# Kernel tuning notes

Measured on AMD Instinct MI355X. Metric: run time of the kernel, lower is better.

## Reference

```python
import jax, jax.numpy as jnp
import numpy as np

LS = (0, 1, 2, 3)                 # spherical-harmonic degrees of edge_attrs
DIMS = [2 * l + 1 for l in LS]    # [1,3,5,7], total 16
OFFS = np.cumsum([0] + DIMS)      # slice offsets into the SH axis
C = 128                           # node feature channels (128x0e)
C_DOWN = 64                       # node_feats_down_irreps = 64x0e
N_BESSEL = 8                      # edge_feats_irreps = 8x0e
AVG_NUM_NEIGHBORS = 10.0


def setup_inputs() -> dict:
    key = jax.random.key(0)
    ks = jax.random.split(key, 14)
    N, E = 10000, 100000
    node_attrs = jax.random.normal(ks[0], (N, 10), jnp.float32)
    node_feats = jax.random.normal(ks[1], (N, C), jnp.float32)
    edge_attrs = jax.random.normal(ks[2], (E, sum(DIMS)), jnp.float32)
    edge_feats = jax.random.normal(ks[3], (E, N_BESSEL), jnp.float32)
    edge_index = jax.random.randint(ks[4], (2, E), 0, N, dtype=jnp.int32)
    inv_c = 1.0 / np.sqrt(C)
    W_up = jax.random.normal(ks[5], (C, C), jnp.float32) * inv_c
    W_down = jax.random.normal(ks[6], (C, C_DOWN), jnp.float32) * inv_c
    W_skip = jax.random.normal(ks[7], (C, C), jnp.float32) * inv_c
    # FullyConnectedNet dims: [8 + 2*64] + 3*[256] + [weight_numel = 4*C]
    dims = [N_BESSEL + 2 * C_DOWN, 256, 256, 256, len(LS) * C]
    W_fc0 = jax.random.normal(ks[8], (dims[0], dims[1]), jnp.float32)
    W_fc1 = jax.random.normal(ks[9], (dims[1], dims[2]), jnp.float32)
    W_fc2 = jax.random.normal(ks[10], (dims[2], dims[3]), jnp.float32)
    W_fc3 = jax.random.normal(ks[11], (dims[3], dims[4]), jnp.float32)
    # final Linear(irreps_mid -> target): independent channel mixing per l
    W_out = jax.random.normal(ks[12], (len(LS), C, C), jnp.float32) * inv_c
    return dict(node_attrs=node_attrs, node_feats=node_feats, edge_attrs=edge_attrs,
                edge_feats=edge_feats, edge_index=edge_index,
                W_up=W_up, W_down=W_down, W_skip=W_skip,
                W_fc0=W_fc0, W_fc1=W_fc1, W_fc2=W_fc2, W_fc3=W_fc3, W_out=W_out)


def reference(node_attrs, node_feats, edge_attrs, edge_feats, edge_index,
              W_up, W_down, W_skip, W_fc0, W_fc1, W_fc2, W_fc3, W_out):
    sender = edge_index[0]
    receiver = edge_index[1]
    N = node_feats.shape[0]

    # skip connection (e3nn Linear on 0e channels)
    sc = node_feats @ W_skip                                   # [N, C]
    x_up = node_feats @ W_up                                   # [N, C]
    x_down = node_feats @ W_down                               # [N, 64]

    # radial weight network on augmented edge features
    aug = jnp.concatenate([edge_feats, x_down[sender], x_down[receiver]], axis=-1)  # [E, 136]
    h = aug
    for W in (W_fc0, W_fc1, W_fc2):
        h = jax.nn.silu(h @ (W / jnp.sqrt(jnp.asarray(W.shape[0], h.dtype))))
    tp_w = h @ (W_fc3 / jnp.sqrt(jnp.asarray(W_fc3.shape[0], h.dtype)))  # [E, 4*C]
    tp_w = tp_w.reshape(-1, len(LS), C)                        # [E, 4, C]

    # per-edge 'uvu' tensor product: 128x0e (gathered sender) x SH(lmax=3)
    xs = x_up[sender]                                          # [E, C]
    parts = []
    for i, l in enumerate(LS):
        Y = edge_attrs[:, OFFS[i]:OFFS[i + 1]]                 # [E, 2l+1]
        cg = 1.0 / np.sqrt(2 * l + 1)                          # w3j(0,l,l)
        part = (tp_w[:, i, :] * xs)[:, :, None] * (Y * cg)[:, None, :]  # [E, C, 2l+1]
        parts.append(part.reshape(part.shape[0], C * (2 * l + 1)))
    mji = jnp.concatenate(parts, axis=-1)                      # [E, C*16]

    # scatter-sum to receivers
    message = jax.ops.segment_sum(mji, receiver, num_segments=N)  # [N, C*16]

    # per-l channel-mixing linear, then / avg_num_neighbors, then reshape_irreps
    outs = []
    off = 0
    for i, l in enumerate(LS):
        d = 2 * l + 1
        blk = message[:, off:off + C * d].reshape(N, C, d)
        outs.append(jnp.einsum('ncd,ck->nkd', blk, W_out[i]))
        off += C * d
    out = jnp.concatenate(outs, axis=-1) / AVG_NUM_NEIGHBORS   # [N, C, 16]
    return out, sc
```

## Files before the change

kernel.cpp:

```cpp
#include <hip/hip_runtime.h>
#include <math.h>

using bf16x8 = __attribute__((ext_vector_type(8))) short;
using f32x4  = __attribute__((ext_vector_type(4))) float;

__device__ __forceinline__ float silu_f(float x) {
    float e = __expf(-x);
    float d = 1.f + e;
    return x * __builtin_amdgcn_rcpf(d);
}

__device__ __forceinline__ unsigned short f2bf(float x) {
    union { float f; unsigned u; } v; v.f = x;
    unsigned u = v.u;
    return (unsigned short)((u + 0x7FFFu + ((u >> 16) & 1u)) >> 16);
}
__device__ __forceinline__ unsigned f2bf2(float lo, float hi) {
    return (unsigned)f2bf(lo) | ((unsigned)f2bf(hi) << 16);
}
__device__ __forceinline__ float bf2f(unsigned short h) {
    union { unsigned u; float f; } v; v.u = ((unsigned)h) << 16;
    return v.f;
}

__global__ __launch_bounds__(256) void k_node_gemm(
    const float* __restrict__ A,
    const float* __restrict__ Wskip, const float* __restrict__ Wup, const float* __restrict__ Wdown,
    float* __restrict__ sc, float* __restrict__ xup, float* __restrict__ xdown, int N)
{
    __shared__ float As[64][129];
    const int t = threadIdx.x;
    const int n0 = blockIdx.x * 64;
    for (int i = t; i < 64 * 32; i += 256) {
        int r = i >> 5, c4 = i & 31;
        int n = n0 + r;
        float4 v = make_float4(0.f, 0.f, 0.f, 0.f);
        if (n < N) v = ((const float4*)(A + (size_t)n * 128))[c4];
        As[r][c4 * 4 + 0] = v.x; As[r][c4 * 4 + 1] = v.y;
        As[r][c4 * 4 + 2] = v.z; As[r][c4 * 4 + 3] = v.w;
    }
    __syncthreads();
    const int tc = t & 15, tr = t >> 4;
    const int col0 = blockIdx.y * 64 + tc * 4;
    const float* W; float* dst; int ldw, wc, ldd;
    if (col0 < 128)      { W = Wskip; ldw = 128; wc = col0;       dst = sc;    ldd = 128; }
    else if (col0 < 256) { W = Wup;   ldw = 128; wc = col0 - 128; dst = xup;   ldd = 128; }
    else                 { W = Wdown; ldw = 64;  wc = col0 - 256; dst = xdown; ldd = 64;  }
    float acc[4][4] = {};
    for (int k = 0; k < 128; k++) {
        float4 wv = *(const float4*)(W + (size_t)k * ldw + wc);
        float wvv[4] = {wv.x, wv.y, wv.z, wv.w};
        float av[4];
        #pragma unroll
        for (int ii = 0; ii < 4; ii++) av[ii] = As[tr * 4 + ii][k];
        #pragma unroll
        for (int ii = 0; ii < 4; ii++)
            #pragma unroll
            for (int jj = 0; jj < 4; jj++)
                acc[ii][jj] = fmaf(av[ii], wvv[jj], acc[ii][jj]);
    }
    #pragma unroll
    for (int ii = 0; ii < 4; ii++) {
        int n = n0 + tr * 4 + ii;
        if (n < N)
            *(float4*)(dst + (size_t)n * ldd + wc) =
                make_float4(acc[ii][0], acc[ii][1], acc[ii][2], acc[ii][3]);
    }
}

__global__ __launch_bounds__(256) void k_prep_w(
    const float* __restrict__ W, unsigned short* __restrict__ Wt,
    int Kin, int Kpad, int Nout, float scale)
{
    int i = blockIdx.x * 256 + threadIdx.x;
    if (i >= Nout * Kpad) return;
    int n = i / Kpad, k = i - n * Kpad;
    float v = (k < Kin) ? W[(size_t)k * Nout + n] * scale : 0.f;
    Wt[i] = f2bf(v);
}

#define MEB 128

__global__ __launch_bounds__(512, 2) void k_mlp_mfma(
    const float* __restrict__ ef, const int* __restrict__ eidx,
    const float* __restrict__ xdown,
    const unsigned short* __restrict__ Wt0, const unsigned short* __restrict__ Wt1,
    const unsigned short* __restrict__ Wt2, const unsigned short* __restrict__ Wt3,
    unsigned short* __restrict__ tp_w, int E, int eLo, int eHi)
{
    __shared__ unsigned short bufA[MEB][264];
    __shared__ unsigned short bufB[MEB][264];
    __shared__ int sE[MEB], rE[MEB];
    const int t = threadIdx.x;
    const int w = t >> 6, lane = t & 63;
    const int rA = lane & 15;
    const int kb = (lane >> 4) * 8;
    const int r0 = (lane >> 4) * 4;
    const int e0 = eLo + blockIdx.x * MEB;

    bf16x8 bw[16];
    f32x4 acc[8][2];

#define LOADW(WT, KPADW, NKS)                                                     \
    _Pragma("unroll")                                                             \
    for (int ks = 0; ks < NKS; ks++)                                              \
        _Pragma("unroll")                                                         \
        for (int nt = 0; nt < 2; nt++)                                            \
            bw[ks * 2 + nt] = *(const bf16x8*)&(WT)[(size_t)(w * 32 + nt * 16 + rA) * (KPADW) + ks * 32 + kb];

#define LMFMA(IN, NKS)                                                            \
    _Pragma("unroll")                                                             \
    for (int mt = 0; mt < 8; mt++)                                                \
        _Pragma("unroll")                                                         \
        for (int nt = 0; nt < 2; nt++)                                            \
            acc[mt][nt] = (f32x4){0.f, 0.f, 0.f, 0.f};                            \
    _Pragma("unroll")                                                             \
    for (int ks = 0; ks < NKS; ks++) {                                            \
        const int kk = ks * 32 + kb;                                              \
        bf16x8 afr[8];                                                            \
        _Pragma("unroll")                                                         \
        for (int mt = 0; mt < 8; mt++)                                            \
            afr[mt] = *(const bf16x8*)&IN[mt * 16 + rA][kk];                      \
        _Pragma("unroll")                                                         \
        for (int mt = 0; mt < 8; mt++)                                            \
            _Pragma("unroll")                                                     \
            for (int nt = 0; nt < 2; nt++)                                        \
                acc[mt][nt] = __builtin_amdgcn_mfma_f32_16x16x32_bf16(afr[mt], bw[ks * 2 + nt], acc[mt][nt], 0, 0, 0); \
    }

#define EPILOG(OUT, DOSILU)                                                       \
    _Pragma("unroll")                                                             \
    for (int mt = 0; mt < 8; mt++)                                                \
        _Pragma("unroll")                                                         \
        for (int nt = 0; nt < 2; nt++) {                                          \
            const int col = w * 32 + nt * 16 + rA;                                \
            _Pragma("unroll")                                                     \
            for (int r = 0; r < 4; r++) {                                         \
                float x = acc[mt][nt][r];                                         \
                if (DOSILU) x = silu_f(x);                                        \
                OUT[mt * 16 + r0 + r][col] = f2bf(x);                             \
            }                                                                     \
        }

    if (t < MEB) {
        int e = e0 + t; if (e >= E) e = E - 1;
        sE[t] = eidx[e]; rE[t] = eidx[E + e];
    }
    __syncthreads();
    for (int i = t; i < MEB * 24; i += 512) {
        int r = i / 24, c = 136 + i % 24;
        bufA[r][c] = 0;
    }
    for (int i = t; i < MEB * 34; i += 512) {
        int e = i / 34, j = i - e * 34;
        float4 v;
        if (j < 2) { int ee = e0 + e; if (ee >= E) ee = E - 1; v = ((const float4*)(ef + (size_t)ee * 8))[j]; }
        else if (j < 18) v = ((const float4*)(xdown + (size_t)sE[e] * 64))[j - 2];
        else             v = ((const float4*)(xdown + (size_t)rE[e] * 64))[j - 18];
        unsigned lo = f2bf2(v.x, v.y), hi = f2bf2(v.z, v.w);
        *(uint2*)&bufA[e][j * 4] = make_uint2(lo, hi);
    }
    __syncthreads();

    LOADW(Wt0, 160, 5)
    LMFMA(bufA, 5)
    EPILOG(bufB, true)
    __syncthreads();

    LOADW(Wt1, 256, 8)
    LMFMA(bufB, 8)
    EPILOG(bufA, true)
    __syncthreads();

    LOADW(Wt2, 256, 8)
    LMFMA(bufA, 8)
    EPILOG(bufB, true)
    __syncthreads();

    LOADW(Wt3, 256, 8)
    LMFMA(bufB, 8)
    EPILOG(bufA, false)
    __syncthreads();
    for (int i = t; i < MEB * 64; i += 512) {
        int r = i >> 6, c4 = i & 63;
        int ee = e0 + r;
        if (ee < eHi) {
            ushort4 hv = *(ushort4*)&bufA[r][c4 * 4];
            *(ushort4*)&tp_w[(size_t)(ee - eLo) * 512 + c4 * 4] = hv;
        }
    }
    __syncthreads();

    LOADW(Wt3 + (size_t)256 * 256, 256, 8)
    LMFMA(bufB, 8)
    EPILOG(bufA, false)
    __syncthreads();
    for (int i = t; i < MEB * 64; i += 512) {
        int r = i >> 6, c4 = i & 63;
        int ee = e0 + r;
        if (ee < eHi) {
            ushort4 hv = *(ushort4*)&bufA[r][c4 * 4];
            *(ushort4*)&tp_w[(size_t)(ee - eLo) * 512 + 256 + c4 * 4] = hv;
        }
    }
#undef LOADW
#undef LMFMA
#undef EPILOG
}

__global__ __launch_bounds__(256, 2) void k_zx(
    unsigned short* __restrict__ tpw, const int* __restrict__ eidx,
    const float* __restrict__ xup, const unsigned short* __restrict__ WoT,
    int E, int eLo, int eHi)
{
    __shared__ __align__(16) unsigned short As[128 * 128];
    __shared__ __align__(16) unsigned short Bs[128 * 128];
    const int t = threadIdx.x;
    const int m0 = blockIdx.x * 128;
    const int l  = blockIdx.y;
    const int nE = eHi - eLo;

    #pragma unroll
    for (int i = 0; i < 8; i++) {
        int idx = i * 256 + t;
        int r = idx >> 4, cc = idx & 15;
        int el = m0 + r;
        int ecl = el < nE ? el : nE - 1;
        int s = eidx[eLo + ecl];
        uint4 tv = *(const uint4*)(tpw + (size_t)ecl * 512 + l * 128 + (cc << 3));
        float4 x0 = *(const float4*)(xup + (size_t)s * 128 + (cc << 3));
        float4 x1 = *(const float4*)(xup + (size_t)s * 128 + (cc << 3) + 4);
        const unsigned short* hp = (const unsigned short*)&tv;
        uint4 ov;
        unsigned* op = (unsigned*)&ov;
        op[0] = f2bf2(bf2f(hp[0]) * x0.x, bf2f(hp[1]) * x0.y);
        op[1] = f2bf2(bf2f(hp[2]) * x0.z, bf2f(hp[3]) * x0.w);
        op[2] = f2bf2(bf2f(hp[4]) * x1.x, bf2f(hp[5]) * x1.y);
        op[3] = f2bf2(bf2f(hp[6]) * x1.z, bf2f(hp[7]) * x1.w);
        *(uint4*)(&As[r * 128 + ((cc ^ (r & 7)) << 3)]) = ov;
    }
    #pragma unroll
    for (int i = 0; i < 8; i++) {
        int idx = i * 256 + t;
        int r = idx >> 4, cc = idx & 15;
        uint4 bv = *(const uint4*)(WoT + ((size_t)l * 128 + r) * 128 + (cc << 3));
        *(uint4*)(&Bs[r * 128 + ((cc ^ (r & 7)) << 3)]) = bv;
    }
    __syncthreads();

    const int lane = t & 63, rA = lane & 15, q = lane >> 4;
    const int wm = (t >> 6) & 1, wn = (t >> 6) >> 1;
    f32x4 acc[4][4];
    #pragma unroll
    for (int mt = 0; mt < 4; mt++)
        #pragma unroll
        for (int nt = 0; nt < 4; nt++)
            acc[mt][nt] = (f32x4){0.f, 0.f, 0.f, 0.f};

    #pragma unroll
    for (int ks = 0; ks < 4; ks++) {
        const int cc = ks * 4 + q;
        bf16x8 af[4], bfr[4];
        #pragma unroll
        for (int mt = 0; mt < 4; mt++) {
            int row = wm * 64 + mt * 16 + rA;
            af[mt] = *(const bf16x8*)&As[row * 128 + ((cc ^ (row & 7)) << 3)];
        }
        #pragma unroll
        for (int nt = 0; nt < 4; nt++) {
            int row = wn * 64 + nt * 16 + rA;
            bfr[nt] = *(const bf16x8*)&Bs[row * 128 + ((cc ^ (row & 7)) << 3)];
        }
        #pragma unroll
        for (int mt = 0; mt < 4; mt++)
            #pragma unroll
            for (int nt = 0; nt < 4; nt++)
                acc[mt][nt] = __builtin_amdgcn_mfma_f32_16x16x32_bf16(af[mt], bfr[nt], acc[mt][nt], 0, 0, 0);
    }
    __syncthreads();

    #pragma unroll
    for (int mt = 0; mt < 4; mt++) {
        #pragma unroll
        for (int r = 0; r < 4; r++) {
            int row = m0 + wm * 64 + mt * 16 + q * 4 + r;
            if (row >= nE) continue;
            #pragma unroll
            for (int nt = 0; nt < 4; nt++) {
                int col = wn * 64 + nt * 16 + rA;
                tpw[(size_t)row * 512 + l * 128 + col] = f2bf(acc[mt][nt][r]);
            }
        }
    }
}

__global__ __launch_bounds__(256) void k_hist(const int* __restrict__ recv, int* __restrict__ deg, int E)
{
    int e = blockIdx.x * 256 + threadIdx.x;
    if (e < E) atomicAdd(&deg[recv[e]], 1);
}

__global__ __launch_bounds__(1024) void k_scan(const int* __restrict__ deg, int* __restrict__ rowptr, int N)
{
    __shared__ int sdata[1024];
    __shared__ int carry;
    const int t = threadIdx.x;
    if (t == 0) carry = 0;
    __syncthreads();
    for (int base = 0; base < N; base += 1024) {
        int i = base + t;
        int v = (i < N) ? deg[i] : 0;
        sdata[t] = v;
        __syncthreads();
        for (int off = 1; off < 1024; off <<= 1) {
            int x = (t >= off) ? sdata[t - off] : 0;
            __syncthreads();
            sdata[t] += x;
            __syncthreads();
        }
        if (i < N) rowptr[i] = carry + sdata[t] - v;
        __syncthreads();
        if (t == 0) carry += sdata[1023];
        __syncthreads();
    }
    if (t == 0) rowptr[N] = carry;
}

__global__ __launch_bounds__(256) void k_scatter(const int* __restrict__ recv,
    const int* __restrict__ rowptr, int* __restrict__ fill, int* __restrict__ perm, int E)
{
    int e = blockIdx.x * 256 + threadIdx.x;
    if (e < E) {
        int r = recv[e];
        int pos = rowptr[r] + atomicAdd(&fill[r], 1);
        perm[pos] = e;
    }
}

__global__ __launch_bounds__(256) void k_sortlists(int* __restrict__ perm, const int* __restrict__ rowptr, int N)
{
    int n = blockIdx.x * 256 + threadIdx.x;
    if (n >= N) return;
    int lo = rowptr[n], hi = rowptr[n + 1];
    for (int i = lo + 1; i < hi; i++) {
        int key = perm[i];
        int j = i - 1;
        while (j >= lo && perm[j] > key) { perm[j + 1] = perm[j]; j--; }
        perm[j + 1] = key;
    }
}

__global__ __launch_bounds__(256) void k_gather(
    const unsigned short* __restrict__ z, const float* __restrict__ ea,
    const int* __restrict__ perm, const int* __restrict__ rowptr,
    float* __restrict__ outb, int E, int eLo, int eHi, int storeMode)
{
    const int n = blockIdx.x;
    const int lo = rowptr[n], hi = rowptr[n + 1];
    const int t = threadIdx.x;
    const int c = t & 127, half = t >> 7;
    constexpr float CG1 = 0.57735026919f, CG2 = 0.44721359550f, CG3 = 0.37796447301f;
    float acc[8] = {};
    __shared__ int eL[64];
    __shared__ float yL[64][17];
    for (int base = lo; base < hi; base += 64) {
        int cnt = min(64, hi - base);
        for (int i = t; i < cnt; i += 256)
            eL[i] = perm[base + i];
        __syncthreads();
        for (int i = t; i < cnt * 16; i += 256) {
            int el = i >> 4, m = i & 15;
            yL[el][m] = ea[(size_t)eL[el] * 16 + m];
        }
        __syncthreads();
        for (int j = 0; j < cnt; j++) {
            int e = eL[j];
            if (e < eLo || e >= eHi) continue;
            const unsigned short* zz = z + (size_t)(e - eLo) * 512;
            const float* y = yL[j];
            if (half == 0) {
                float z0 = bf2f(zz[c]);
                float z1 = bf2f(zz[128 + c]) * CG1;
                float z2 = bf2f(zz[256 + c]) * CG2;
                acc[0] = fmaf(z0, y[0], acc[0]);
                #pragma unroll
                for (int m = 0; m < 3; m++) acc[1 + m] = fmaf(z1, y[1 + m], acc[1 + m]);
                #pragma unroll
                for (int m = 0; m < 4; m++) acc[4 + m] = fmaf(z2, y[4 + m], acc[4 + m]);
            } else {
                float z2 = bf2f(zz[256 + c]) * CG2;
                float z3 = bf2f(zz[384 + c]) * CG3;
                acc[0] = fmaf(z2, y[8], acc[0]);
                #pragma unroll
                for (int m = 0; m < 7; m++) acc[1 + m] = fmaf(z3, y[9 + m], acc[1 + m]);
            }
        }
        __syncthreads();
    }
    float* orow = outb + (size_t)n * 2048 + (size_t)c * 16 + half * 8;
    if (storeMode) {
        *(float4*)orow       = make_float4(acc[0], acc[1], acc[2], acc[3]);
        *(float4*)(orow + 4) = make_float4(acc[4], acc[5], acc[6], acc[7]);
    } else {
        float4 a = *(float4*)orow, b = *(float4*)(orow + 4);
        a.x += acc[0]; a.y += acc[1]; a.z += acc[2]; a.w += acc[3];
        b.x += acc[4]; b.y += acc[5]; b.z += acc[6]; b.w += acc[7];
        *(float4*)orow = a; *(float4*)(orow + 4) = b;
    }
}

extern "C" void kernel_launch(void* const* d_in, const int* in_sizes, int n_in,
                              void* d_out, int out_size, void* d_ws, size_t ws_size,
                              hipStream_t stream)
{
    const float* node_feats = (const float*)d_in[1];
    const float* edge_attrs = (const float*)d_in[2];
    const float* edge_feats = (const float*)d_in[3];
    const int*   edge_index = (const int*)d_in[4];
    const float* W_up   = (const float*)d_in[5];
    const float* W_down = (const float*)d_in[6];
    const float* W_skip = (const float*)d_in[7];
    const float* W_fc0  = (const float*)d_in[8];
    const float* W_fc1  = (const float*)d_in[9];
    const float* W_fc2  = (const float*)d_in[10];
    const float* W_fc3  = (const float*)d_in[11];
    const float* W_out  = (const float*)d_in[12];
    const int N = in_sizes[1] / 128;
    const int E = in_sizes[3] / 8;

    float* out = (float*)d_out;
    float* sc  = out + (size_t)N * 2048;

    float* xup   = (float*)d_ws;
    float* xdown = xup + (size_t)N * 128;
    int* deg    = (int*)(xdown + (size_t)N * 64);
    int* fill   = deg + N;
    int* rowptr = fill + N;
    int* perm   = rowptr + N + 1;
    size_t used = (size_t)((char*)(perm + E) - (char*)d_ws);
    used = (used + 255) & ~(size_t)255;
    unsigned short* Wt0 = (unsigned short*)((char*)d_ws + used);
    unsigned short* Wt1 = Wt0 + 256 * 160;
    unsigned short* Wt2 = Wt1 + 256 * 256;
    unsigned short* Wt3 = Wt2 + 256 * 256;
    unsigned short* WoT = Wt3 + 512 * 256;
    used = (size_t)((char*)(WoT + 4 * 128 * 128) - (char*)d_ws);
    used = (used + 255) & ~(size_t)255;
    unsigned short* tpw = (unsigned short*)((char*)d_ws + used);
    size_t avail = (ws_size > used) ? ws_size - used : 0;
    long long Ec_l = (long long)(avail / (512 * sizeof(unsigned short)));
    int Ec = (int)(Ec_l > E ? E : Ec_l);
    if (Ec < 8) Ec = 8;
    const int nchunks = (E + Ec - 1) / Ec;

    hipMemsetAsync(deg, 0, (size_t)2 * N * sizeof(int), stream);
    if (nchunks > 1)
        hipMemsetAsync(out, 0, (size_t)N * 2048 * sizeof(float), stream);

    dim3 g1((N + 63) / 64, 5);
    k_node_gemm<<<g1, 256, 0, stream>>>(node_feats, W_skip, W_up, W_down, sc, xup, xdown, N);

    constexpr float S0 = 0.085749292571254f;
    k_prep_w<<<(256 * 160 + 255) / 256, 256, 0, stream>>>(W_fc0, Wt0, 136, 160, 256, S0);
    k_prep_w<<<(256 * 256 + 255) / 256, 256, 0, stream>>>(W_fc1, Wt1, 256, 256, 256, 0.0625f);
    k_prep_w<<<(256 * 256 + 255) / 256, 256, 0, stream>>>(W_fc2, Wt2, 256, 256, 256, 0.0625f);
    k_prep_w<<<(512 * 256 + 255) / 256, 256, 0, stream>>>(W_fc3, Wt3, 256, 256, 512, 0.0625f);
    for (int l = 0; l < 4; l++)
        k_prep_w<<<(128 * 128 + 255) / 256, 256, 0, stream>>>(W_out + (size_t)l * 16384,
                                                              WoT + (size_t)l * 16384,
                                                              128, 128, 128, 0.1f);

    const int* recv = edge_index + E;
    k_hist<<<(E + 255) / 256, 256, 0, stream>>>(recv, deg, E);
    k_scan<<<1, 1024, 0, stream>>>(deg, rowptr, N);
    k_scatter<<<(E + 255) / 256, 256, 0, stream>>>(recv, rowptr, fill, perm, E);
    k_sortlists<<<(N + 255) / 256, 256, 0, stream>>>(perm, rowptr, N);

    for (int ch = 0; ch < nchunks; ch++) {
        int eLo = ch * Ec;
        int eHi = eLo + Ec; if (eHi > E) eHi = E;
        int nE = eHi - eLo;

        k_mlp_mfma<<<(nE + MEB - 1) / MEB, 512, 0, stream>>>(edge_feats, edge_index, xdown,
                                                             Wt0, Wt1, Wt2, Wt3,
                                                             tpw, E, eLo, eHi);
        k_zx<<<dim3((nE + 127) / 128, 4), 256, 0, stream>>>(tpw, edge_index, xup, WoT,
                                                            E, eLo, eHi);
        k_gather<<<N, 256, 0, stream>>>(tpw, edge_attrs, perm, rowptr,
                                        out, E, eLo, eHi, nchunks == 1 ? 1 : 0);
    }
}
```

Measured before the change: 365.1 us.

## Fuse per-edge x_up product and W_out mixing into the MLP kernel

```diff
diff --git a/kernel.cpp b/kernel.cpp
--- a/kernel.cpp
+++ b/kernel.cpp
@@ -83,10 +83,11 @@
 
 __global__ __launch_bounds__(512, 2) void k_mlp_mfma(
     const float* __restrict__ ef, const int* __restrict__ eidx,
-    const float* __restrict__ xdown,
+    const float* __restrict__ xdown, const float* __restrict__ xup,
     const unsigned short* __restrict__ Wt0, const unsigned short* __restrict__ Wt1,
     const unsigned short* __restrict__ Wt2, const unsigned short* __restrict__ Wt3,
-    unsigned short* __restrict__ tp_w, int E, int eLo, int eHi)
+    const unsigned short* __restrict__ WoT,
+    unsigned short* __restrict__ z, int E, int eLo, int eHi)
 {
     __shared__ unsigned short bufA[MEB][264];
     __shared__ unsigned short bufB[MEB][264];
@@ -177,121 +178,70 @@
     EPILOG(bufB, true)
     __syncthreads();
 
-    LOADW(Wt3, 256, 8)
-    LMFMA(bufB, 8)
-    EPILOG(bufA, false)
-    __syncthreads();
-    for (int i = t; i < MEB * 64; i += 512) {
-        int r = i >> 6, c4 = i & 63;
-        int ee = e0 + r;
-        if (ee < eHi) {
-            ushort4 hv = *(ushort4*)&bufA[r][c4 * 4];
-            *(ushort4*)&tp_w[(size_t)(ee - eLo) * 512 + c4 * 4] = hv;
-        }
-    }
-    __syncthreads();
-
-    LOADW(Wt3 + (size_t)256 * 256, 256, 8)
-    LMFMA(bufB, 8)
-    EPILOG(bufA, false)
-    __syncthreads();
-    for (int i = t; i < MEB * 64; i += 512) {
-        int r = i >> 6, c4 = i & 63;
-        int ee = e0 + r;
-        if (ee < eHi) {
-            ushort4 hv = *(ushort4*)&bufA[r][c4 * 4];
-            *(ushort4*)&tp_w[(size_t)(ee - eLo) * 512 + 256 + c4 * 4] = hv;
-        }
+    const float4* __restrict__ xupv = (const float4*)xup;
+    const int l_loc = w >> 2;
+    const int kbase = (w & 3) * 32;
+
+    #pragma unroll
+    for (int p = 0; p < 2; p++) {
+        LOADW(Wt3 + (size_t)p * 256 * 256, 256, 8)
+        LMFMA(bufB, 8)
+        EPILOG(bufA, false)
+        __syncthreads();
+
+        for (int i = t; i < MEB * 64; i += 512) {
+            int e = i >> 6, q = i & 63;
+            float4 v = xupv[(size_t)sE[e] * 32 + (q & 31)];
+            ushort4 hv = *(ushort4*)&bufA[e][q * 4];
+            unsigned lo = f2bf2(bf2f(hv.x) * v.x, bf2f(hv.y) * v.y);
+            unsigned hi = f2bf2(bf2f(hv.z) * v.z, bf2f(hv.w) * v.w);
+            *(uint2*)&bufA[e][q * 4] = make_uint2(lo, hi);
+        }
+        __syncthreads();
+
+        const int l = p * 2 + l_loc;
+        #pragma unroll
+        for (int mt = 0; mt < 8; mt++)
+            #pragma unroll
+            for (int nt = 0; nt < 2; nt++)
+                acc[mt][nt] = (f32x4){0.f, 0.f, 0.f, 0.f};
+        #pragma unroll
+        for (int ks = 0; ks < 4; ks++)
+            #pragma unroll
+            for (int nt = 0; nt < 2; nt++)
+                bw[ks * 2 + nt] = *(const bf16x8*)&WoT[((size_t)l * 128 + kbase + nt * 16 + rA) * 128 + ks * 32 + kb];
+        #pragma unroll
+        for (int ks = 0; ks < 4; ks++) {
+            const int kk = ks * 32 + kb;
+            bf16x8 afr[8];
+            #pragma unroll
+            for (int mt = 0; mt < 8; mt++)
+                afr[mt] = *(const bf16x8*)&bufA[mt * 16 + rA][l_loc * 128 + kk];
+            #pragma unroll
+            for (int mt = 0; mt < 8; mt++)
+                #pragma unroll
+                for (int nt = 0; nt < 2; nt++)
+                    acc[mt][nt] = __builtin_amdgcn_mfma_f32_16x16x32_bf16(afr[mt], bw[ks * 2 + nt], acc[mt][nt], 0, 0, 0);
+        }
+        #pragma unroll
+        for (int mt = 0; mt < 8; mt++) {
+            #pragma unroll
+            for (int r = 0; r < 4; r++) {
+                int ee = e0 + mt * 16 + r0 + r;
+                if (ee < eHi) {
+                    #pragma unroll
+                    for (int nt = 0; nt < 2; nt++) {
+                        int k = kbase + nt * 16 + rA;
+                        z[(size_t)(ee - eLo) * 512 + l * 128 + k] = f2bf(acc[mt][nt][r]);
+                    }
+                }
+            }
+        }
+        __syncthreads();
     }
 #undef LOADW
 #undef LMFMA
 #undef EPILOG
-}
-
-__global__ __launch_bounds__(256, 2) void k_zx(
-    unsigned short* __restrict__ tpw, const int* __restrict__ eidx,
-    const float* __restrict__ xup, const unsigned short* __restrict__ WoT,
-    int E, int eLo, int eHi)
-{
-    __shared__ __align__(16) unsigned short As[128 * 128];
-    __shared__ __align__(16) unsigned short Bs[128 * 128];
-    const int t = threadIdx.x;
-    const int m0 = blockIdx.x * 128;
-    const int l  = blockIdx.y;
-    const int nE = eHi - eLo;
-
-    #pragma unroll
-    for (int i = 0; i < 8; i++) {
-        int idx = i * 256 + t;
-        int r = idx >> 4, cc = idx & 15;
-        int el = m0 + r;
-        int ecl = el < nE ? el : nE - 1;
-        int s = eidx[eLo + ecl];
-        uint4 tv = *(const uint4*)(tpw + (size_t)ecl * 512 + l * 128 + (cc << 3));
-        float4 x0 = *(const float4*)(xup + (size_t)s * 128 + (cc << 3));
-        float4 x1 = *(const float4*)(xup + (size_t)s * 128 + (cc << 3) + 4);
-        const unsigned short* hp = (const unsigned short*)&tv;
-        uint4 ov;
-        unsigned* op = (unsigned*)&ov;
-        op[0] = f2bf2(bf2f(hp[0]) * x0.x, bf2f(hp[1]) * x0.y);
-        op[1] = f2bf2(bf2f(hp[2]) * x0.z, bf2f(hp[3]) * x0.w);
-        op[2] = f2bf2(bf2f(hp[4]) * x1.x, bf2f(hp[5]) * x1.y);
-        op[3] = f2bf2(bf2f(hp[6]) * x1.z, bf2f(hp[7]) * x1.w);
-        *(uint4*)(&As[r * 128 + ((cc ^ (r & 7)) << 3)]) = ov;
-    }
-    #pragma unroll
-    for (int i = 0; i < 8; i++) {
-        int idx = i * 256 + t;
-        int r = idx >> 4, cc = idx & 15;
-        uint4 bv = *(const uint4*)(WoT + ((size_t)l * 128 + r) * 128 + (cc << 3));
-        *(uint4*)(&Bs[r * 128 + ((cc ^ (r & 7)) << 3)]) = bv;
-    }
-    __syncthreads();
-
-    const int lane = t & 63, rA = lane & 15, q = lane >> 4;
-    const int wm = (t >> 6) & 1, wn = (t >> 6) >> 1;
-    f32x4 acc[4][4];
-    #pragma unroll
-    for (int mt = 0; mt < 4; mt++)
-        #pragma unroll
-        for (int nt = 0; nt < 4; nt++)
-            acc[mt][nt] = (f32x4){0.f, 0.f, 0.f, 0.f};
-
-    #pragma unroll
-    for (int ks = 0; ks < 4; ks++) {
-        const int cc = ks * 4 + q;
-        bf16x8 af[4], bfr[4];
-        #pragma unroll
-        for (int mt = 0; mt < 4; mt++) {
-            int row = wm * 64 + mt * 16 + rA;
-            af[mt] = *(const bf16x8*)&As[row * 128 + ((cc ^ (row & 7)) << 3)];
-        }
-        #pragma unroll
-        for (int nt = 0; nt < 4; nt++) {
-            int row = wn * 64 + nt * 16 + rA;
-            bfr[nt] = *(const bf16x8*)&Bs[row * 128 + ((cc ^ (row & 7)) << 3)];
-        }
-        #pragma unroll
-        for (int mt = 0; mt < 4; mt++)
-            #pragma unroll
-            for (int nt = 0; nt < 4; nt++)
-                acc[mt][nt] = __builtin_amdgcn_mfma_f32_16x16x32_bf16(af[mt], bfr[nt], acc[mt][nt], 0, 0, 0);
-    }
-    __syncthreads();
-
-    #pragma unroll
-    for (int mt = 0; mt < 4; mt++) {
-        #pragma unroll
-        for (int r = 0; r < 4; r++) {
-            int row = m0 + wm * 64 + mt * 16 + q * 4 + r;
-            if (row >= nE) continue;
-            #pragma unroll
-            for (int nt = 0; nt < 4; nt++) {
-                int col = wn * 64 + nt * 16 + rA;
-                tpw[(size_t)row * 512 + l * 128 + col] = f2bf(acc[mt][nt][r]);
-            }
-        }
-    }
 }
 
 __global__ __launch_bounds__(256) void k_hist(const int* __restrict__ recv, int* __restrict__ deg, int E)
@@ -446,7 +396,7 @@
     unsigned short* WoT = Wt3 + 512 * 256;
     used = (size_t)((char*)(WoT + 4 * 128 * 128) - (char*)d_ws);
     used = (used + 255) & ~(size_t)255;
-    unsigned short* tpw = (unsigned short*)((char*)d_ws + used);
+    unsigned short* zbuf = (unsigned short*)((char*)d_ws + used);
     size_t avail = (ws_size > used) ? ws_size - used : 0;
     long long Ec_l = (long long)(avail / (512 * sizeof(unsigned short)));
     int Ec = (int)(Ec_l > E ? E : Ec_l);
@@ -481,12 +431,10 @@
         int eHi = eLo + Ec; if (eHi > E) eHi = E;
         int nE = eHi - eLo;
 
-        k_mlp_mfma<<<(nE + MEB - 1) / MEB, 512, 0, stream>>>(edge_feats, edge_index, xdown,
-                                                             Wt0, Wt1, Wt2, Wt3,
-                                                             tpw, E, eLo, eHi);
-        k_zx<<<dim3((nE + 127) / 128, 4), 256, 0, stream>>>(tpw, edge_index, xup, WoT,
-                                                            E, eLo, eHi);
-        k_gather<<<N, 256, 0, stream>>>(tpw, edge_attrs, perm, rowptr,
+        k_mlp_mfma<<<(nE + MEB - 1) / MEB, 512, 0, stream>>>(edge_feats, edge_index, xdown, xup,
+                                                             Wt0, Wt1, Wt2, Wt3, WoT,
+                                                             zbuf, E, eLo, eHi);
+        k_gather<<<N, 256, 0, stream>>>(zbuf, edge_attrs, perm, rowptr,
                                         out, E, eLo, eHi, nchunks == 1 ? 1 : 0);
     }
 }
```

Result: no change. 372.0 us (+1.9%).
